# Kernel optimization log

Measured on AMD Instinct MI355X. Metric: run time of the kernel, lower is better.

Reference implementation:

```python
import jax, jax.numpy as jnp
from jax import lax
import numpy as np

B, L, NQ, NL, NC = 2048, 2048, 8, 3, 3  # batch, signal length, qubits, q-layers, classes


def setup_inputs() -> dict:
    key = jax.random.key(0)
    ks = jax.random.split(key, 20)
    rn = lambda k, shape, s=1.0: jax.random.normal(k, shape, jnp.float32) * s
    return dict(
        x_ecg=rn(ks[0], (B, 1, L)), x_eda=rn(ks[1], (B, 1, L)),
        x_emg=rn(ks[2], (B, 1, L)), x_resp=rn(ks[3], (B, 1, L)),
        conv1_w=rn(ks[4], (4, 16, 1, 3), 0.3), conv1_b=rn(ks[5], (4, 16), 0.05),
        conv2_w=rn(ks[6], (4, 32, 16, 3), 0.1), conv2_b=rn(ks[7], (4, 32), 0.05),
        lstm_w_ih=rn(ks[8], (4, 128, 32), 0.1), lstm_w_hh=rn(ks[9], (4, 128, 32), 0.1),
        lstm_b_ih=rn(ks[10], (4, 128), 0.05), lstm_b_hh=rn(ks[11], (4, 128), 0.05),
        bott_w=rn(ks[12], (8, 128), 0.08), bott_b=rn(ks[13], (8,), 0.05),
        q_weights=rn(ks[14], (NL, NQ, 3)),
        clf_w=rn(ks[15], (NC, 8), 0.3), clf_b=rn(ks[16], (NC,), 0.05),
    )


def _branch(x, c1w, c1b, c2w, c2b, wih, whh, bih, bhh):
    # x: [B,1,L]  ->  h_n: [B,32]
    dn = ('NCH', 'OIH', 'NCH')
    h = lax.conv_general_dilated(x, c1w, (1,), [(1, 1)], dimension_numbers=dn) + c1b[None, :, None]
    h = jax.nn.relu(h)
    h = h.reshape(h.shape[0], h.shape[1], -1, 2).max(-1)  # maxpool k=2
    h = lax.conv_general_dilated(h, c2w, (1,), [(1, 1)], dimension_numbers=dn) + c2b[None, :, None]
    h = jax.nn.relu(h)
    h = h.reshape(h.shape[0], h.shape[1], -1, 2).max(-1)  # [B,32,L//4]
    seq = jnp.swapaxes(h, 1, 2)  # [B,T,32]
    Bn, H = seq.shape[0], whh.shape[1]

    def step(carry, xt):
        hprev, cprev = carry
        gates = xt @ wih.T + hprev @ whh.T + bih + bhh  # [B,4H], torch gate order i,f,g,o
        i, f, g, o = jnp.split(gates, 4, axis=-1)
        c = jax.nn.sigmoid(f) * cprev + jax.nn.sigmoid(i) * jnp.tanh(g)
        hn = jax.nn.sigmoid(o) * jnp.tanh(c)
        return (hn, c), None

    init = (jnp.zeros((Bn, H), seq.dtype), jnp.zeros((Bn, H), seq.dtype))
    (h_n, _), _ = lax.scan(step, init, jnp.swapaxes(seq, 0, 1))
    return h_n


def _apply_1q(psi, gate, q, n):
    # psi: [B, 2^n]; gate: [2,2] (shared) or [B,2,2] (per-sample)
    Bn = psi.shape[0]
    left, right = 2 ** q, 2 ** (n - q - 1)
    s = psi.reshape(Bn, left, 2, right)
    if gate.ndim == 2:
        s = jnp.einsum('ij,bljr->blir', gate, s)
    else:
        s = jnp.einsum('bij,bljr->blir', gate, s)
    return s.reshape(Bn, -1)


def _apply_cnot(psi, c, t, n):
    # c < t always here
    Bn = psi.shape[0]
    s = psi.reshape(Bn, 2 ** c, 2, 2 ** (t - c - 1), 2, 2 ** (n - t - 1))
    s = s.at[:, :, 1].set(jnp.flip(s[:, :, 1], axis=3))
    return s.reshape(Bn, -1)


def _rz(a):
    e = jnp.exp(-0.5j * a)
    z = jnp.zeros_like(e)
    return jnp.stack([jnp.stack([e, z]), jnp.stack([z, jnp.conj(e)])])


def _ry(a):
    c, s = jnp.cos(a / 2), jnp.sin(a / 2)
    return jnp.stack([jnp.stack([c, -s]), jnp.stack([s, c])]).astype(jnp.complex64)


def _quantum(compressed, q_weights):
    # batched 8-qubit statevector simulation; compressed: [B, NQ]
    n = NQ
    Bn = compressed.shape[0]
    angles = compressed * jnp.pi
    psi = jnp.zeros((Bn, 2 ** n), jnp.complex64).at[:, 0].set(1.0)
    c, s = jnp.cos(angles / 2), jnp.sin(angles / 2)
    for q in range(n):  # RX embedding, per-sample gates
        g = jnp.stack([jnp.stack([c[:, q], -1j * s[:, q]], -1),
                       jnp.stack([-1j * s[:, q], c[:, q]], -1)], -2)  # [B,2,2]
        psi = _apply_1q(psi, g, q, n)
    for l in range(q_weights.shape[0]):
        for q in range(n):
            w = q_weights[l, q]
            # pennylane Rot(phi,theta,omega) = RZ(omega) @ RY(theta) @ RZ(phi)
            g = _rz(w[2]) @ _ry(w[1]) @ _rz(w[0])
            psi = _apply_1q(psi, g, q, n)
        stride = l + 1
        for q in range(n):
            t = q + stride
            if t < n:
                psi = _apply_cnot(psi, q, t, n)
    p = (jnp.abs(psi) ** 2).reshape((Bn,) + (2,) * n)
    zs = []
    for i in range(n):  # <Z_i> = P(|0>_i) - P(|1>_i)
        axes = tuple(a for a in range(1, n + 1) if a != i + 1)
        m = p.sum(axes)
        zs.append(m[:, 0] - m[:, 1])
    return jnp.stack(zs, -1).astype(jnp.float32)


def reference(x_ecg, x_eda, x_emg, x_resp, conv1_w, conv1_b, conv2_w, conv2_b,
              lstm_w_ih, lstm_w_hh, lstm_b_ih, lstm_b_hh, bott_w, bott_b,
              q_weights, clf_w, clf_b):
    xs = jnp.stack([x_ecg, x_eda, x_emg, x_resp])  # [4,B,1,L]
    feats = jax.vmap(_branch)(xs, conv1_w, conv1_b, conv2_w, conv2_b,
                              lstm_w_ih, lstm_w_hh, lstm_b_ih, lstm_b_hh)  # [4,B,32]
    combined = jnp.transpose(feats, (1, 0, 2)).reshape(feats.shape[1], -1)  # [B,128]
    compressed = jnp.tanh(combined @ bott_w.T + bott_b)  # [B,8]
    q_out = _quantum(compressed, q_weights)  # [B,8]
    logits = q_out @ clf_w.T + clf_b  # [B,3]
    return logits
```

## Files before the change

kernel.cpp:

```cpp
#include <hip/hip_runtime.h>
#include <hip/hip_bf16.h>

#define BATCH 2048
#define LSIG 2048
#define TSTEPS 512
#define CH 16
#define NCHUNK (TSTEPS / CH)

typedef float v2f __attribute__((ext_vector_type(2)));
typedef float v4f __attribute__((ext_vector_type(4)));
typedef __bf16 b16x8 __attribute__((ext_vector_type(8)));
typedef float f32x4 __attribute__((ext_vector_type(4)));

#define PKFMA(d, a, b) asm("v_pk_fma_f32 %0, %1, %2, %0" : "+v"(d) : "v"(a), "v"(b))

__device__ __forceinline__ float sigf(float x) {
    return __fdividef(1.f, 1.f + __expf(-x));
}
__device__ __forceinline__ float tanhfast(float x) {
    return 1.f - __fdividef(2.f, __expf(2.f * x) + 1.f);
}
__device__ __forceinline__ unsigned short bf16rne(float f) {
    unsigned u = __float_as_uint(f);
    return (unsigned short)((u + 0x7FFFu + ((u >> 16) & 1u)) >> 16);
}
__device__ __forceinline__ int swz(int co) {
    return (co < 16) ? ((co >> 2) * 8 + (co & 3))
                     : (((co >> 2) - 4) * 8 + 4 + (co & 3));
}

__global__ __launch_bounds__(64) void frontend_kernel(
    const float* __restrict__ x0, const float* __restrict__ x1,
    const float* __restrict__ x2, const float* __restrict__ x3,
    const float* __restrict__ c1w, const float* __restrict__ c1b,
    const float* __restrict__ c2w, const float* __restrict__ c2b,
    unsigned short* __restrict__ seqh, unsigned short* __restrict__ seql,
    int t0, int Tseg)
{
    const int s    = blockIdx.x;
    const int br   = blockIdx.y & 3;
    const int ck   = blockIdx.y >> 2;
    const int lane = threadIdx.x;
    const float* xg = (br == 0) ? x0 : (br == 1) ? x1 : (br == 2) ? x2 : x3;

    __shared__ float xs_c[70];
    __shared__ float p1buf[34][16];

    const int ci = lane & 15;
    const int co = lane & 31;
    const int hf = lane >> 5;
    const int sp = swz(co);
    const int tc0 = t0 + ck * CH;
    const int lt0 = ck * CH;

    const float w10 = c1w[br * 48 + ci * 3 + 0];
    const float w11 = c1w[br * 48 + ci * 3 + 1];
    const float w12 = c1w[br * 48 + ci * 3 + 2];
    const float b1v = c1b[br * 16 + ci];

    float wt[24];
    {
        const v4f* p = (const v4f*)(c2w + br * 1536 + co * 48 + hf * 24);
        #pragma unroll
        for (int i = 0; i < 6; ++i) ((v4f*)wt)[i] = p[i];
    }
    v4f w2p[3][2];
    #pragma unroll
    for (int k = 0; k < 3; ++k)
        #pragma unroll
        for (int h2 = 0; h2 < 2; ++h2)
            w2p[k][h2] = (v4f){ wt[(h2 * 4 + 0) * 3 + k], wt[(h2 * 4 + 1) * 3 + k],
                                wt[(h2 * 4 + 2) * 3 + k], wt[(h2 * 4 + 3) * 3 + k] };
    const float b2v = c2b[br * 32 + co];

    {
        int g = 4 * tc0 - 3 + lane;
        xs_c[lane] = ((unsigned)g < (unsigned)LSIG) ? xg[(size_t)s * LSIG + g] : 0.f;
        if (lane < 6) {
            int g2 = 4 * tc0 + 61 + lane;
            xs_c[64 + lane] = ((unsigned)g2 < (unsigned)LSIG) ? xg[(size_t)s * LSIG + g2] : 0.f;
        }
    }
    __syncthreads();

    #pragma unroll 1
    for (int it = 0; it < 9; ++it) {
        int idx = it * 64 + lane;
        if (idx < 34 * 16) {
            int pl = idx >> 4;
            float xa = xs_c[2 * pl + 0], xb = xs_c[2 * pl + 1];
            float xc = xs_c[2 * pl + 2], xd = xs_c[2 * pl + 3];
            float a0 = fmaf(xc, w12, fmaf(xb, w11, fmaf(xa, w10, b1v)));
            float a1 = fmaf(xd, w12, fmaf(xc, w11, fmaf(xb, w10, b1v)));
            float v = fmaxf(fmaxf(a0, a1), 0.f);
            int p1g = 2 * tc0 - 1 + pl;
            v = ((unsigned)p1g < (unsigned)(LSIG / 2)) ? v : 0.f;
            p1buf[pl][idx & 15] = v;
        }
    }
    __syncthreads();

    {
        const v4f* pbase = (const v4f*)&p1buf[0][0];
        const int h2o = hf * 2;
        v4f r0a = pbase[0 * 4 + h2o], r0b = pbase[0 * 4 + h2o + 1];
        v4f r1a = pbase[1 * 4 + h2o], r1b = pbase[1 * 4 + h2o + 1];
        v4f r2a = pbase[2 * 4 + h2o], r2b = pbase[2 * 4 + h2o + 1];
        v4f r3a = pbase[3 * 4 + h2o], r3b = pbase[3 * 4 + h2o + 1];
        #pragma unroll 1
        for (int tl = 0; tl < CH; ++tl) {
            v2f aA = {0.f, 0.f}, aB = {0.f, 0.f};
            PKFMA(aA, r0a.xy, w2p[0][0].xy); PKFMA(aA, r0a.zw, w2p[0][0].zw);
            PKFMA(aA, r0b.xy, w2p[0][1].xy); PKFMA(aA, r0b.zw, w2p[0][1].zw);
            PKFMA(aA, r1a.xy, w2p[1][0].xy); PKFMA(aA, r1a.zw, w2p[1][0].zw);
            PKFMA(aA, r1b.xy, w2p[1][1].xy); PKFMA(aA, r1b.zw, w2p[1][1].zw);
            PKFMA(aA, r2a.xy, w2p[2][0].xy); PKFMA(aA, r2a.zw, w2p[2][0].zw);
            PKFMA(aA, r2b.xy, w2p[2][1].xy); PKFMA(aA, r2b.zw, w2p[2][1].zw);
            PKFMA(aB, r1a.xy, w2p[0][0].xy); PKFMA(aB, r1a.zw, w2p[0][0].zw);
            PKFMA(aB, r1b.xy, w2p[0][1].xy); PKFMA(aB, r1b.zw, w2p[0][1].zw);
            PKFMA(aB, r2a.xy, w2p[1][0].xy); PKFMA(aB, r2a.zw, w2p[1][0].zw);
            PKFMA(aB, r2b.xy, w2p[1][1].xy); PKFMA(aB, r2b.zw, w2p[1][1].zw);
            PKFMA(aB, r3a.xy, w2p[2][0].xy); PKFMA(aB, r3a.zw, w2p[2][0].zw);
            PKFMA(aB, r3b.xy, w2p[2][1].xy); PKFMA(aB, r3b.zw, w2p[2][1].zw);
            float sA = aA.x + aA.y, sB = aB.x + aB.y;
            sA += __shfl_xor(sA, 32);
            sB += __shfl_xor(sB, 32);
            float sv = fmaxf(fmaxf(sA, sB) + b2v, 0.f);
            unsigned short hb = bf16rne(sv);
            float hif = __uint_as_float(((unsigned)hb) << 16);
            unsigned short lb = bf16rne(sv - hif);
            size_t off = (((size_t)br * Tseg + (lt0 + tl)) * 2048 + s) * 32 + sp;
            if (hf == 0) seqh[off] = hb;
            else         seql[off] = lb;
            r0a = r2a; r0b = r2b; r1a = r3a; r1b = r3b;
            if (tl < CH - 1) {
                r2a = pbase[(2 * tl + 4) * 4 + h2o]; r2b = pbase[(2 * tl + 4) * 4 + h2o + 1];
                r3a = pbase[(2 * tl + 5) * 4 + h2o]; r3b = pbase[(2 * tl + 5) * 4 + h2o + 1];
            }
        }
    }
}

__global__ __launch_bounds__(64, 1) void lstm_mfma_kernel(
    const unsigned short* __restrict__ seqh, const unsigned short* __restrict__ seql,
    const float* __restrict__ wih, const float* __restrict__ whh,
    const float* __restrict__ bih, const float* __restrict__ bhh,
    float* __restrict__ state, float* __restrict__ feats,
    int t0, int Tseg)
{
    const int s0   = blockIdx.x * 16;
    const int br   = blockIdx.y;
    const int lane = threadIdx.x;
    const int c    = lane & 15;
    const int q    = lane >> 4;

    __shared__ f32x4 bias_lds[8][64];

    #pragma unroll
    for (int n = 0; n < 8; ++n) {
        f32x4 b;
        #pragma unroll
        for (int r = 0; r < 4; ++r) {
            int g = 16 * n + 4 * q + r;
            b[r] = bih[br * 128 + g] + bhh[br * 128 + g];
        }
        bias_lds[n][lane] = b;
    }

    b16x8 wihhi[8], wihlo[8], whhhi[8], whhlo[8];
    #pragma unroll
    for (int n = 0; n < 8; ++n) {
        const int gr = 16 * n + c;
        const float* pi = wih + (size_t)br * 4096 + (size_t)gr * 32;
        const float* ph = whh + (size_t)br * 4096 + (size_t)gr * 32;
        v4f ia = *(const v4f*)(pi + 4 * q);
        v4f ib = *(const v4f*)(pi + 16 + 4 * q);
        v4f ha = *(const v4f*)(ph + 4 * q);
        v4f hb = *(const v4f*)(ph + 16 + 4 * q);
        #pragma unroll
        for (int j = 0; j < 4; ++j) {
            __bf16 t;
            t = (__bf16)ia[j]; wihhi[n][j]     = t; wihlo[n][j]     = (__bf16)(ia[j] - (float)t);
            t = (__bf16)ib[j]; wihhi[n][4 + j] = t; wihlo[n][4 + j] = (__bf16)(ib[j] - (float)t);
            t = (__bf16)ha[j]; whhhi[n][j]     = t; whhlo[n][j]     = (__bf16)(ha[j] - (float)t);
            t = (__bf16)hb[j]; whhhi[n][4 + j] = t; whhlo[n][4 + j] = (__bf16)(hb[j] - (float)t);
        }
    }

    b16x8 bhh_f, bhl_f;
    float cst[2][4];
    if (t0 == 0) {
        #pragma unroll
        for (int j = 0; j < 8; ++j) { bhh_f[j] = (__bf16)0.f; bhl_f[j] = (__bf16)0.f; }
        #pragma unroll
        for (int hh = 0; hh < 2; ++hh)
            #pragma unroll
            for (int r = 0; r < 4; ++r) cst[hh][r] = 0.f;
    } else {
        const float* st = state + (((size_t)br * BATCH + s0 + c) * 2) * 32;
        #pragma unroll
        for (int hh = 0; hh < 2; ++hh)
            #pragma unroll
            for (int r = 0; r < 4; ++r) {
                int u = 16 * hh + 4 * q + r;
                float hv = st[u];
                __bf16 hb2 = (__bf16)hv;
                bhh_f[hh * 4 + r] = hb2;
                bhl_f[hh * 4 + r] = (__bf16)(hv - (float)hb2);
                cst[hh][r] = st[32 + u];
            }
    }
    __syncthreads();

    size_t rowe = (((size_t)br * Tseg + 0) * 2048 + s0 + c) * 32 + (size_t)q * 8;
    b16x8 bxh = *reinterpret_cast<const b16x8*>(seqh + rowe);
    b16x8 bxl = *reinterpret_cast<const b16x8*>(seql + rowe);

    #pragma unroll 1
    for (int t = 0; t < Tseg; ++t) {
        b16x8 nxh = bxh, nxl = bxl;
        if (t < Tseg - 1) {
            size_t re = (((size_t)br * Tseg + (t + 1)) * 2048 + s0 + c) * 32 + (size_t)q * 8;
            nxh = *reinterpret_cast<const b16x8*>(seqh + re);
            nxl = *reinterpret_cast<const b16x8*>(seql + re);
        }

        f32x4 acc[8];
        #pragma unroll
        for (int n = 0; n < 8; ++n) acc[n] = bias_lds[n][lane];
        #pragma unroll
        for (int n = 0; n < 8; ++n) {
            acc[n] = __builtin_amdgcn_mfma_f32_16x16x32_bf16(whhhi[n], bhh_f, acc[n], 0, 0, 0);
            acc[n] = __builtin_amdgcn_mfma_f32_16x16x32_bf16(whhhi[n], bhl_f, acc[n], 0, 0, 0);
            acc[n] = __builtin_amdgcn_mfma_f32_16x16x32_bf16(whhlo[n], bhh_f, acc[n], 0, 0, 0);
            acc[n] = __builtin_amdgcn_mfma_f32_16x16x32_bf16(wihhi[n], bxh,   acc[n], 0, 0, 0);
            acc[n] = __builtin_amdgcn_mfma_f32_16x16x32_bf16(wihhi[n], bxl,   acc[n], 0, 0, 0);
            acc[n] = __builtin_amdgcn_mfma_f32_16x16x32_bf16(wihlo[n], bxh,   acc[n], 0, 0, 0);
        }

        const bool last = (t0 + t == TSTEPS - 1);
        #pragma unroll
        for (int hh = 0; hh < 2; ++hh) {
            #pragma unroll
            for (int r = 0; r < 4; ++r) {
                float gi = acc[0 + hh][r];
                float gf = acc[2 + hh][r];
                float gg = acc[4 + hh][r];
                float go = acc[6 + hh][r];
                float si = sigf(gi);
                float sf = sigf(gf);
                float tg = tanhfast(gg);
                float so = sigf(go);
                float cc = fmaf(sf, cst[hh][r], si * tg);
                cst[hh][r] = cc;
                float hv = so * tanhfast(cc);
                __bf16 hb2 = (__bf16)hv;
                bhh_f[hh * 4 + r] = hb2;
                bhl_f[hh * 4 + r] = (__bf16)(hv - (float)hb2);
                if (last)
                    feats[((size_t)br * BATCH + s0 + c) * 32 + 16 * hh + 4 * q + r] = hv;
            }
        }
        bxh = nxh; bxl = nxl;
    }

    if (t0 + Tseg < TSTEPS) {
        float* st = state + (((size_t)br * BATCH + s0 + c) * 2) * 32;
        #pragma unroll
        for (int hh = 0; hh < 2; ++hh)
            #pragma unroll
            for (int r = 0; r < 4; ++r) {
                int u = 16 * hh + 4 * q + r;
                st[u]      = (float)bhh_f[hh * 4 + r] + (float)bhl_f[hh * 4 + r];
                st[32 + u] = cst[hh][r];
            }
    }
}

__global__ __launch_bounds__(64, 2) void branch_fallback(
    const float* __restrict__ x0, const float* __restrict__ x1,
    const float* __restrict__ x2, const float* __restrict__ x3,
    const float* __restrict__ c1w, const float* __restrict__ c1b,
    const float* __restrict__ c2w, const float* __restrict__ c2b,
    const float* __restrict__ wih, const float* __restrict__ whh,
    const float* __restrict__ bih, const float* __restrict__ bhh,
    float* __restrict__ feats)
{
    const int s    = blockIdx.x;
    const int br   = blockIdx.y;
    const int lane = threadIdx.x;
    const float* xg = (br == 0) ? x0 : (br == 1) ? x1 : (br == 2) ? x2 : x3;

    __shared__ float xs_c[70];
    __shared__ float p1buf[34][16];
    __shared__ float seqb[CH][32];
    __shared__ float hb[2][32];

    const int ci = lane & 15;
    const int co = lane & 31;
    const int hf = lane >> 5;

    const float bs0 = bih[br * 128 + lane]      + bhh[br * 128 + lane];
    const float bs1 = bih[br * 128 + lane + 64] + bhh[br * 128 + lane + 64];

    if (lane < 32) hb[0][lane] = 0.f;
    float c_state = 0.f;

    #pragma unroll 1
    for (int chk = 0; chk < NCHUNK; ++chk) {
        const int tc0 = chk * CH;
        {
            int g = 4 * tc0 - 3 + lane;
            xs_c[lane] = ((unsigned)g < (unsigned)LSIG) ? xg[(size_t)s * LSIG + g] : 0.f;
            if (lane < 6) {
                int g2 = 4 * tc0 + 61 + lane;
                xs_c[64 + lane] = ((unsigned)g2 < (unsigned)LSIG) ? xg[(size_t)s * LSIG + g2] : 0.f;
            }
        }
        const float* pc1 = c1w + br * 48 + ci * 3;  asm volatile("" : "+v"(pc1));
        const float w10 = pc1[0], w11 = pc1[1], w12 = pc1[2];
        const float* pb1 = c1b + br * 16 + ci;      asm volatile("" : "+v"(pb1));
        const float b1v = pb1[0];
        const float* pc2 = c2w + br * 1536 + co * 48 + hf * 24;
        asm volatile("" : "+v"(pc2));
        float wt[24];
        #pragma unroll
        for (int i = 0; i < 6; ++i) ((v4f*)wt)[i] = ((const v4f*)pc2)[i];
        v4f w2p[3][2];
        #pragma unroll
        for (int k = 0; k < 3; ++k)
            #pragma unroll
            for (int h2 = 0; h2 < 2; ++h2)
                w2p[k][h2] = (v4f){ wt[(h2 * 4 + 0) * 3 + k], wt[(h2 * 4 + 1) * 3 + k],
                                    wt[(h2 * 4 + 2) * 3 + k], wt[(h2 * 4 + 3) * 3 + k] };
        const float* pb2 = c2b + br * 32 + co;      asm volatile("" : "+v"(pb2));
        const float b2v = pb2[0];
        __syncthreads();
        #pragma unroll 1
        for (int it = 0; it < 9; ++it) {
            int idx = it * 64 + lane;
            if (idx < 34 * 16) {
                int pl = idx >> 4;
                float xa = xs_c[2 * pl + 0], xb = xs_c[2 * pl + 1];
                float xc = xs_c[2 * pl + 2], xd = xs_c[2 * pl + 3];
                float a0 = fmaf(xc, w12, fmaf(xb, w11, fmaf(xa, w10, b1v)));
                float a1 = fmaf(xd, w12, fmaf(xc, w11, fmaf(xb, w10, b1v)));
                float v = fmaxf(fmaxf(a0, a1), 0.f);
                int p1g = 2 * tc0 - 1 + pl;
                v = ((unsigned)p1g < (unsigned)(LSIG / 2)) ? v : 0.f;
                p1buf[pl][idx & 15] = v;
            }
        }
        __syncthreads();
        {
            const v4f* pbase = (const v4f*)&p1buf[0][0];
            const int h2o = hf * 2;
            v4f r0a = pbase[0 * 4 + h2o], r0b = pbase[0 * 4 + h2o + 1];
            v4f r1a = pbase[1 * 4 + h2o], r1b = pbase[1 * 4 + h2o + 1];
            v4f r2a = pbase[2 * 4 + h2o], r2b = pbase[2 * 4 + h2o + 1];
            v4f r3a = pbase[3 * 4 + h2o], r3b = pbase[3 * 4 + h2o + 1];
            #pragma unroll 1
            for (int tl = 0; tl < CH; ++tl) {
                v2f aA = {0.f, 0.f}, aB = {0.f, 0.f};
                PKFMA(aA, r0a.xy, w2p[0][0].xy); PKFMA(aA, r0a.zw, w2p[0][0].zw);
                PKFMA(aA, r0b.xy, w2p[0][1].xy); PKFMA(aA, r0b.zw, w2p[0][1].zw);
                PKFMA(aA, r1a.xy, w2p[1][0].xy); PKFMA(aA, r1a.zw, w2p[1][0].zw);
                PKFMA(aA, r1b.xy, w2p[1][1].xy); PKFMA(aA, r1b.zw, w2p[1][1].zw);
                PKFMA(aA, r2a.xy, w2p[2][0].xy); PKFMA(aA, r2a.zw, w2p[2][0].zw);
                PKFMA(aA, r2b.xy, w2p[2][1].xy); PKFMA(aA, r2b.zw, w2p[2][1].zw);
                PKFMA(aB, r1a.xy, w2p[0][0].xy); PKFMA(aB, r1a.zw, w2p[0][0].zw);
                PKFMA(aB, r1b.xy, w2p[0][1].xy); PKFMA(aB, r1b.zw, w2p[0][1].zw);
                PKFMA(aB, r2a.xy, w2p[1][0].xy); PKFMA(aB, r2a.zw, w2p[1][0].zw);
                PKFMA(aB, r2b.xy, w2p[1][1].xy); PKFMA(aB, r2b.zw, w2p[1][1].zw);
                PKFMA(aB, r3a.xy, w2p[2][0].xy); PKFMA(aB, r3a.zw, w2p[2][0].zw);
                PKFMA(aB, r3b.xy, w2p[2][1].xy); PKFMA(aB, r3b.zw, w2p[2][1].zw);
                float sA = aA.x + aA.y, sB = aB.x + aB.y;
                sA += __shfl_xor(sA, 32);
                sB += __shfl_xor(sB, 32);
                if (hf == 0)
                    seqb[tl][co] = fmaxf(fmaxf(sA, sB) + b2v, 0.f);
                r0a = r2a; r0b = r2b; r1a = r3a; r1b = r3b;
                if (tl < CH - 1) {
                    r2a = pbase[(2 * tl + 4) * 4 + h2o]; r2b = pbase[(2 * tl + 4) * 4 + h2o + 1];
                    r3a = pbase[(2 * tl + 5) * 4 + h2o]; r3b = pbase[(2 * tl + 5) * 4 + h2o + 1];
                }
            }
        }
        __syncthreads();
        float gpx0[CH], gpx1[CH];
        {
            const float* pwi = wih + (size_t)br * 4096 + (size_t)lane * 32;
            asm volatile("" : "+v"(pwi));
            v4f wiA[8], wiB[8];
            #pragma unroll
            for (int j = 0; j < 8; ++j) {
                wiA[j] = ((const v4f*)pwi)[j];
                wiB[j] = ((const v4f*)(pwi + 64 * 32))[j];
            }
            #pragma unroll
            for (int tl = 0; tl < CH; ++tl) {
                const v4f* xq = (const v4f*)&seqb[tl][0];
                v2f aA = {0.f, 0.f}, aB = {0.f, 0.f};
                #pragma unroll
                for (int j = 0; j < 8; ++j) {
                    v4f xv = xq[j];
                    PKFMA(aA, xv.xy, wiA[j].xy); PKFMA(aA, xv.zw, wiA[j].zw);
                    PKFMA(aB, xv.xy, wiB[j].xy); PKFMA(aB, xv.zw, wiB[j].zw);
                }
                gpx0[tl] = aA.x + aA.y;
                gpx1[tl] = aB.x + aB.y;
            }
        }
        {
            const float* pwh = whh + (size_t)br * 4096 + (size_t)lane * 32;
            asm volatile("" : "+v"(pwh));
            v4f whA[8], whB[8];
            #pragma unroll
            for (int j = 0; j < 8; ++j) {
                whA[j] = ((const v4f*)pwh)[j];
                whB[j] = ((const v4f*)(pwh + 64 * 32))[j];
            }
            #pragma unroll
            for (int tl = 0; tl < CH; ++tl) {
                __syncthreads();
                const int p = (tc0 + tl) & 1;
                const v4f* hq = (const v4f*)&hb[p][0];
                v2f aA = {0.f, 0.f}, aB = {0.f, 0.f};
                #pragma unroll
                for (int j = 0; j < 8; ++j) {
                    v4f hv = hq[j];
                    PKFMA(aA, hv.xy, whA[j].xy); PKFMA(aA, hv.zw, whA[j].zw);
                    PKFMA(aB, hv.xy, whB[j].xy); PKFMA(aB, hv.zw, whB[j].zw);
                }
                float g0 = bs0 + gpx0[tl] + aA.x + aA.y;
                float g1 = bs1 + gpx1[tl] + aB.x + aB.y;
                float a0 = sigf(g0);
                float earg = (lane < 32) ? 2.f * g1 : -g1;
                float e1 = __expf(fminf(earg, 80.f));
                float num = (lane < 32) ? e1 - 1.f : 1.f;
                float a1 = __fdividef(num, e1 + 1.f);
                float fa = __shfl_xor(a0, 32);
                float oa = __shfl_xor(a1, 32);
                if (lane < 32) {
                    c_state = fmaf(fa, c_state, a0 * a1);
                    hb[p ^ 1][lane] = oa * tanhfast(c_state);
                }
            }
        }
    }
    __syncthreads();
    if (lane < 32)
        feats[((size_t)br * BATCH + s) * 32 + lane] = hb[0][lane];
}


__device__ __forceinline__ void apply1q(float2* psi, int lane, int q,
                                        float2 g00, float2 g01,
                                        float2 g10, float2 g11)
{
    const int shift = 7 - q;
    const int right = 1 << shift;
    #pragma unroll
    for (int pp = 0; pp < 2; ++pp) {
        int p  = lane + 64 * pp;
        int l  = p >> shift;
        int r  = p & (right - 1);
        int i0 = (l << (shift + 1)) + r;
        int i1 = i0 + right;
        float2 a = psi[i0], b = psi[i1];
        float2 n0 = make_float2(g00.x * a.x - g00.y * a.y + g01.x * b.x - g01.y * b.y,
                                g00.x * a.y + g00.y * a.x + g01.x * b.y + g01.y * b.x);
        float2 n1 = make_float2(g10.x * a.x - g10.y * a.y + g11.x * b.x - g11.y * b.y,
                                g10.x * a.y + g10.y * a.x + g11.x * b.y + g11.y * b.x);
        psi[i0] = n0;
        psi[i1] = n1;
    }
    __syncthreads();
}

__global__ __launch_bounds__(64) void tail_kernel(
    const float* __restrict__ feats, const float* __restrict__ bw,
    const float* __restrict__ bb, const float* __restrict__ qw,
    const float* __restrict__ cw, const float* __restrict__ cb,
    float* __restrict__ out)
{
    const int s    = blockIdx.x;
    const int lane = threadIdx.x;

    __shared__ float comb[128];
    __shared__ float2 psi[256];
    __shared__ float ang[8];

    comb[lane]      = feats[(size_t)(lane >> 5) * (BATCH * 32) + (size_t)s * 32 + (lane & 31)];
    comb[lane + 64] = feats[(size_t)((lane + 64) >> 5) * (BATCH * 32) + (size_t)s * 32 + (lane & 31)];
    __syncthreads();

    {
        int q = lane >> 3, k0 = lane & 7;
        float p = 0.f;
        #pragma unroll
        for (int i = 0; i < 16; ++i) {
            int k = k0 + 8 * i;
            p = fmaf(comb[k], bw[q * 128 + k], p);
        }
        p += __shfl_xor(p, 4);
        p += __shfl_xor(p, 2);
        p += __shfl_xor(p, 1);
        if (k0 == 0) ang[q] = tanhf(p + bb[q]);
    }
    #pragma unroll
    for (int r = 0; r < 4; ++r) {
        int idx = lane + 64 * r;
        psi[idx] = make_float2(idx == 0 ? 1.f : 0.f, 0.f);
    }
    __syncthreads();

    const float PI_F = 3.14159265358979323846f;

    for (int q = 0; q < 8; ++q) {
        float half = ang[q] * PI_F * 0.5f;
        float cv = cosf(half), sv = sinf(half);
        apply1q(psi, lane, q,
                make_float2(cv, 0.f), make_float2(0.f, -sv),
                make_float2(0.f, -sv), make_float2(cv, 0.f));
    }

    for (int l = 0; l < 3; ++l) {
        for (int q = 0; q < 8; ++q) {
            float phi = qw[(l * 8 + q) * 3 + 0];
            float th  = qw[(l * 8 + q) * 3 + 1];
            float om  = qw[(l * 8 + q) * 3 + 2];
            float ct = cosf(0.5f * th), st = sinf(0.5f * th);
            float A = 0.5f * (phi + om), D = 0.5f * (phi - om);
            float cA = cosf(A), sA = sinf(A), cD = cosf(D), sD = sinf(D);
            apply1q(psi, lane, q,
                    make_float2(ct * cA, -ct * sA), make_float2(-st * cD, -st * sD),
                    make_float2(st * cD, -st * sD), make_float2(ct * cA,  ct * sA));
        }
        int stride = l + 1;
        for (int q = 0; q + stride < 8; ++q) {
            int cbit = 1 << (7 - q);
            int tbit = 1 << (7 - (q + stride));
            #pragma unroll
            for (int r = 0; r < 4; ++r) {
                int idx = lane + 64 * r;
                if ((idx & cbit) && !(idx & tbit)) {
                    int j = idx | tbit;
                    float2 tmp = psi[idx];
                    psi[idx] = psi[j];
                    psi[j] = tmp;
                }
            }
            __syncthreads();
        }
    }

    float z[8];
    #pragma unroll
    for (int q = 0; q < 8; ++q) z[q] = 0.f;
    #pragma unroll
    for (int r = 0; r < 4; ++r) {
        int idx = lane + 64 * r;
        float2 a = psi[idx];
        float pr = a.x * a.x + a.y * a.y;
        #pragma unroll
        for (int q = 0; q < 8; ++q)
            z[q] += (idx & (1 << (7 - q))) ? -pr : pr;
    }
    #pragma unroll
    for (int q = 0; q < 8; ++q) {
        #pragma unroll
        for (int off = 32; off; off >>= 1) z[q] += __shfl_xor(z[q], off);
    }
    if (lane == 0) {
        #pragma unroll
        for (int c = 0; c < 3; ++c) {
            float acc = cb[c];
            #pragma unroll
            for (int q = 0; q < 8; ++q) acc = fmaf(z[q], cw[c * 8 + q], acc);
            out[s * 3 + c] = acc;
        }
    }
}

extern "C" void kernel_launch(void* const* d_in, const int* in_sizes, int n_in,
                              void* d_out, int out_size, void* d_ws, size_t ws_size,
                              hipStream_t stream)
{
    (void)in_sizes; (void)n_in; (void)out_size;
    const float* x0  = (const float*)d_in[0];
    const float* x1  = (const float*)d_in[1];
    const float* x2  = (const float*)d_in[2];
    const float* x3  = (const float*)d_in[3];
    const float* c1w = (const float*)d_in[4];
    const float* c1b = (const float*)d_in[5];
    const float* c2w = (const float*)d_in[6];
    const float* c2b = (const float*)d_in[7];
    const float* wih = (const float*)d_in[8];
    const float* whh = (const float*)d_in[9];
    const float* bih = (const float*)d_in[10];
    const float* bhh = (const float*)d_in[11];
    const float* bw  = (const float*)d_in[12];
    const float* bb  = (const float*)d_in[13];
    const float* qw  = (const float*)d_in[14];
    const float* cw  = (const float*)d_in[15];
    const float* cb  = (const float*)d_in[16];

    const size_t state_b = 4ULL * BATCH * 64ULL * 4ULL;
    const size_t feats_b = 4ULL * BATCH * 32ULL * 4ULL;
    const size_t per_t   = 4ULL * 2048ULL * 32ULL * 4ULL;

    int Tseg = 0;
    for (int cand = 512; cand >= 32; cand >>= 1) {
        if ((size_t)cand * per_t + state_b + feats_b <= ws_size) { Tseg = cand; break; }
    }

    if (Tseg > 0) {
        size_t seg_elems = (size_t)Tseg * 4ULL * 2048ULL * 32ULL;
        unsigned short* seqh = (unsigned short*)d_ws;
        unsigned short* seql = seqh + seg_elems;
        float* state = (float*)((char*)d_ws + 2ULL * seg_elems * 2ULL);
        float* feats = (float*)((char*)state + state_b);

        for (int t0 = 0; t0 < TSTEPS; t0 += Tseg) {
            frontend_kernel<<<dim3(BATCH, 4 * (Tseg / CH)), 64, 0, stream>>>(
                x0, x1, x2, x3, c1w, c1b, c2w, c2b, seqh, seql, t0, Tseg);
            lstm_mfma_kernel<<<dim3(BATCH / 16, 4), 64, 0, stream>>>(
                seqh, seql, wih, whh, bih, bhh, state, feats, t0, Tseg);
        }
        tail_kernel<<<BATCH, 64, 0, stream>>>(
            feats, bw, bb, qw, cw, cb, (float*)d_out);
    } else {
        float* feats = (float*)d_ws;
        branch_fallback<<<dim3(BATCH, 4), 64, 0, stream>>>(
            x0, x1, x2, x3, c1w, c1b, c2w, c2b, wih, whh, bih, bhh, feats);
        tail_kernel<<<BATCH, 64, 0, stream>>>(
            feats, bw, bb, qw, cw, cb, (float*)d_out);
    }
}
```

Baseline: 1.490 ms.

## Split LSTM gate computation across two waves with LDS exchange

Each LSTM block now runs two wavefronts, each owning four of the eight gate tiles. The waves apply their gate activations locally and swap results through double-buffered shared memory with one barrier per step. Both waves then redundantly compute the cell and hidden updates. The input projection for the next step is computed after the current step's update, taking it off the recurrent critical path. This halves the MFMA and transcendental work per wave on the serial recurrence, in exchange for a per-step barrier and extra LDS traffic.

Result: slower. 1.776 ms (+19.2%).

```diff
diff --git a/kernel.cpp b/kernel.cpp
--- a/kernel.cpp
+++ b/kernel.cpp
@@ -141,7 +141,7 @@
     }
 }
 
-__global__ __launch_bounds__(64, 1) void lstm_mfma_kernel(
+__global__ __launch_bounds__(128, 1) void lstm_mfma_kernel(
     const unsigned short* __restrict__ seqh, const unsigned short* __restrict__ seql,
     const float* __restrict__ wih, const float* __restrict__ whh,
     const float* __restrict__ bih, const float* __restrict__ bhh,
@@ -150,26 +150,19 @@
 {
     const int s0   = blockIdx.x * 16;
     const int br   = blockIdx.y;
-    const int lane = threadIdx.x;
+    const int tid  = threadIdx.x;
+    const int w    = tid >> 6;
+    const int lane = tid & 63;
     const int c    = lane & 15;
     const int q    = lane >> 4;
 
-    __shared__ f32x4 bias_lds[8][64];
-
+    __shared__ f32x4 ex[2][2][4][64];
+
+    b16x8 wihhi[4], wihlo[4], whhhi[4], whhlo[4];
+    f32x4 bias[4];
     #pragma unroll
-    for (int n = 0; n < 8; ++n) {
-        f32x4 b;
-        #pragma unroll
-        for (int r = 0; r < 4; ++r) {
-            int g = 16 * n + 4 * q + r;
-            b[r] = bih[br * 128 + g] + bhh[br * 128 + g];
-        }
-        bias_lds[n][lane] = b;
-    }
-
-    b16x8 wihhi[8], wihlo[8], whhhi[8], whhlo[8];
-    #pragma unroll
-    for (int n = 0; n < 8; ++n) {
+    for (int m = 0; m < 4; ++m) {
+        const int n = 4 * w + m;
         const int gr = 16 * n + c;
         const float* pi = wih + (size_t)br * 4096 + (size_t)gr * 32;
         const float* ph = whh + (size_t)br * 4096 + (size_t)gr * 32;
@@ -179,11 +172,16 @@
         v4f hb = *(const v4f*)(ph + 16 + 4 * q);
         #pragma unroll
         for (int j = 0; j < 4; ++j) {
-            __bf16 t;
-            t = (__bf16)ia[j]; wihhi[n][j]     = t; wihlo[n][j]     = (__bf16)(ia[j] - (float)t);
-            t = (__bf16)ib[j]; wihhi[n][4 + j] = t; wihlo[n][4 + j] = (__bf16)(ib[j] - (float)t);
-            t = (__bf16)ha[j]; whhhi[n][j]     = t; whhlo[n][j]     = (__bf16)(ha[j] - (float)t);
-            t = (__bf16)hb[j]; whhhi[n][4 + j] = t; whhlo[n][4 + j] = (__bf16)(hb[j] - (float)t);
+            __bf16 tt;
+            tt = (__bf16)ia[j]; wihhi[m][j]     = tt; wihlo[m][j]     = (__bf16)(ia[j] - (float)tt);
+            tt = (__bf16)ib[j]; wihhi[m][4 + j] = tt; wihlo[m][4 + j] = (__bf16)(ib[j] - (float)tt);
+            tt = (__bf16)ha[j]; whhhi[m][j]     = tt; whhlo[m][j]     = (__bf16)(ha[j] - (float)tt);
+            tt = (__bf16)hb[j]; whhhi[m][4 + j] = tt; whhlo[m][4 + j] = (__bf16)(hb[j] - (float)tt);
+        }
+        #pragma unroll
+        for (int r = 0; r < 4; ++r) {
+            int g = 16 * n + 4 * q + r;
+            bias[m][r] = bih[br * 128 + g] + bhh[br * 128 + g];
         }
     }
 
@@ -210,61 +208,94 @@
                 cst[hh][r] = st[32 + u];
             }
     }
-    __syncthreads();
-
-    size_t rowe = (((size_t)br * Tseg + 0) * 2048 + s0 + c) * 32 + (size_t)q * 8;
-    b16x8 bxh = *reinterpret_cast<const b16x8*>(seqh + rowe);
-    b16x8 bxl = *reinterpret_cast<const b16x8*>(seql + rowe);
+
+    f32x4 xacc[4];
+    {
+        size_t rowe = (((size_t)br * Tseg + 0) * 2048 + s0 + c) * 32 + (size_t)q * 8;
+        b16x8 bxh = *reinterpret_cast<const b16x8*>(seqh + rowe);
+        b16x8 bxl = *reinterpret_cast<const b16x8*>(seql + rowe);
+        #pragma unroll
+        for (int m = 0; m < 4; ++m) {
+            xacc[m] = __builtin_amdgcn_mfma_f32_16x16x32_bf16(wihhi[m], bxh, bias[m], 0, 0, 0);
+            xacc[m] = __builtin_amdgcn_mfma_f32_16x16x32_bf16(wihhi[m], bxl, xacc[m], 0, 0, 0);
+            xacc[m] = __builtin_amdgcn_mfma_f32_16x16x32_bf16(wihlo[m], bxh, xacc[m], 0, 0, 0);
+        }
+    }
 
     #pragma unroll 1
     for (int t = 0; t < Tseg; ++t) {
-        b16x8 nxh = bxh, nxl = bxl;
-        if (t < Tseg - 1) {
+        b16x8 nxh, nxl;
+        const bool more = (t < Tseg - 1);
+        if (more) {
             size_t re = (((size_t)br * Tseg + (t + 1)) * 2048 + s0 + c) * 32 + (size_t)q * 8;
             nxh = *reinterpret_cast<const b16x8*>(seqh + re);
             nxl = *reinterpret_cast<const b16x8*>(seql + re);
         }
 
-        f32x4 acc[8];
-        #pragma unroll
-        for (int n = 0; n < 8; ++n) acc[n] = bias_lds[n][lane];
-        #pragma unroll
-        for (int n = 0; n < 8; ++n) {
-            acc[n] = __builtin_amdgcn_mfma_f32_16x16x32_bf16(whhhi[n], bhh_f, acc[n], 0, 0, 0);
-            acc[n] = __builtin_amdgcn_mfma_f32_16x16x32_bf16(whhhi[n], bhl_f, acc[n], 0, 0, 0);
-            acc[n] = __builtin_amdgcn_mfma_f32_16x16x32_bf16(whhlo[n], bhh_f, acc[n], 0, 0, 0);
-            acc[n] = __builtin_amdgcn_mfma_f32_16x16x32_bf16(wihhi[n], bxh,   acc[n], 0, 0, 0);
-            acc[n] = __builtin_amdgcn_mfma_f32_16x16x32_bf16(wihhi[n], bxl,   acc[n], 0, 0, 0);
-            acc[n] = __builtin_amdgcn_mfma_f32_16x16x32_bf16(wihlo[n], bxh,   acc[n], 0, 0, 0);
-        }
+        f32x4 acc[4];
+        #pragma unroll
+        for (int m = 0; m < 4; ++m) {
+            acc[m] = __builtin_amdgcn_mfma_f32_16x16x32_bf16(whhhi[m], bhh_f, xacc[m], 0, 0, 0);
+            acc[m] = __builtin_amdgcn_mfma_f32_16x16x32_bf16(whhhi[m], bhl_f, acc[m], 0, 0, 0);
+            acc[m] = __builtin_amdgcn_mfma_f32_16x16x32_bf16(whhlo[m], bhh_f, acc[m], 0, 0, 0);
+        }
+
+        f32x4 a[4];
+        if (w == 0) {
+            #pragma unroll
+            for (int m = 0; m < 4; ++m)
+                #pragma unroll
+                for (int r = 0; r < 4; ++r) a[m][r] = sigf(acc[m][r]);
+        } else {
+            #pragma unroll
+            for (int m = 0; m < 2; ++m)
+                #pragma unroll
+                for (int r = 0; r < 4; ++r) a[m][r] = tanhfast(acc[m][r]);
+            #pragma unroll
+            for (int m = 2; m < 4; ++m)
+                #pragma unroll
+                for (int r = 0; r < 4; ++r) a[m][r] = sigf(acc[m][r]);
+        }
+
+        const int par = t & 1;
+        #pragma unroll
+        for (int m = 0; m < 4; ++m) ex[par][w][m][lane] = a[m];
+        __syncthreads();
+        f32x4 ob[4];
+        #pragma unroll
+        for (int m = 0; m < 4; ++m) ob[m] = ex[par][w ^ 1][m][lane];
 
         const bool last = (t0 + t == TSTEPS - 1);
+        const f32x4* P = (w == 0) ? a : ob;
+        const f32x4* Q = (w == 0) ? ob : a;
         #pragma unroll
         for (int hh = 0; hh < 2; ++hh) {
             #pragma unroll
             for (int r = 0; r < 4; ++r) {
-                float gi = acc[0 + hh][r];
-                float gf = acc[2 + hh][r];
-                float gg = acc[4 + hh][r];
-                float go = acc[6 + hh][r];
-                float si = sigf(gi);
-                float sf = sigf(gf);
-                float tg = tanhfast(gg);
-                float so = sigf(go);
-                float cc = fmaf(sf, cst[hh][r], si * tg);
+                float vi = P[hh][r], vf = P[2 + hh][r];
+                float vg = Q[hh][r], vo = Q[2 + hh][r];
+                float cc = fmaf(vf, cst[hh][r], vi * vg);
                 cst[hh][r] = cc;
-                float hv = so * tanhfast(cc);
+                float hv = vo * tanhfast(cc);
                 __bf16 hb2 = (__bf16)hv;
                 bhh_f[hh * 4 + r] = hb2;
                 bhl_f[hh * 4 + r] = (__bf16)(hv - (float)hb2);
-                if (last)
+                if (last && w == 0)
                     feats[((size_t)br * BATCH + s0 + c) * 32 + 16 * hh + 4 * q + r] = hv;
             }
         }
-        bxh = nxh; bxl = nxl;
-    }
-
-    if (t0 + Tseg < TSTEPS) {
+
+        if (more) {
+            #pragma unroll
+            for (int m = 0; m < 4; ++m) {
+                xacc[m] = __builtin_amdgcn_mfma_f32_16x16x32_bf16(wihhi[m], nxh, bias[m], 0, 0, 0);
+                xacc[m] = __builtin_amdgcn_mfma_f32_16x16x32_bf16(wihhi[m], nxl, xacc[m], 0, 0, 0);
+                xacc[m] = __builtin_amdgcn_mfma_f32_16x16x32_bf16(wihlo[m], nxh, xacc[m], 0, 0, 0);
+            }
+        }
+    }
+
+    if (w == 0 && t0 + Tseg < TSTEPS) {
         float* st = state + (((size_t)br * BATCH + s0 + c) * 2) * 32;
         #pragma unroll
         for (int hh = 0; hh < 2; ++hh)
@@ -625,7 +656,7 @@
         for (int t0 = 0; t0 < TSTEPS; t0 += Tseg) {
             frontend_kernel<<<dim3(BATCH, 4 * (Tseg / CH)), 64, 0, stream>>>(
                 x0, x1, x2, x3, c1w, c1b, c2w, c2b, seqh, seql, t0, Tseg);
-            lstm_mfma_kernel<<<dim3(BATCH / 16, 4), 64, 0, stream>>>(
+            lstm_mfma_kernel<<<dim3(BATCH / 16, 4), 128, 0, stream>>>(
                 seqh, seql, wih, whh, bih, bhh, state, feats, t0, Tseg);
         }
         tail_kernel<<<BATCH, 64, 0, stream>>>(
```

## Interleave two independent LSTM batch tiles per wave to overlap MFMA and activations

Applied to the files above, without the earlier changes.

Each LSTM wave now processes two 16-sample tiles instead of one. The MFMA gate chain of one tile is interleaved with the sigmoid/tanh cell update of the other, so matrix and transcendental work from independent recurrences can overlap and hide the serial dependency latency. The grid is halved (BATCH/32 blocks), which lowers wave-level parallelism and raises register pressure with two accumulator sets and two states. The per-gate MFMA order also now puts the input-projection terms before the recurrent ones, so they do not depend on the previous hidden state.

Result: slower. 2.523 ms (+69.4%).

```diff
diff --git a/kernel.cpp b/kernel.cpp
--- a/kernel.cpp
+++ b/kernel.cpp
@@ -141,6 +141,44 @@
     }
 }
 
+#define GATE_CHAINS(ACC, XH, XL, HH, HL)                                        \
+    {                                                                           \
+        _Pragma("unroll")                                                       \
+        for (int n = 0; n < 8; ++n) {                                           \
+            f32x4 a_ = bias_lds[n][lane];                                       \
+            a_ = __builtin_amdgcn_mfma_f32_16x16x32_bf16(wihhi[n], XH, a_, 0, 0, 0); \
+            a_ = __builtin_amdgcn_mfma_f32_16x16x32_bf16(wihhi[n], XL, a_, 0, 0, 0); \
+            a_ = __builtin_amdgcn_mfma_f32_16x16x32_bf16(wihlo[n], XH, a_, 0, 0, 0); \
+            a_ = __builtin_amdgcn_mfma_f32_16x16x32_bf16(whhhi[n], HH, a_, 0, 0, 0); \
+            a_ = __builtin_amdgcn_mfma_f32_16x16x32_bf16(whhhi[n], HL, a_, 0, 0, 0); \
+            a_ = __builtin_amdgcn_mfma_f32_16x16x32_bf16(whhlo[n], HH, a_, 0, 0, 0); \
+            ACC[n] = a_;                                                        \
+        }                                                                       \
+    }
+
+#define ADVANCE(ACC, HH, HL, CS, LAST, FP)                                      \
+    {                                                                           \
+        _Pragma("unroll")                                                       \
+        for (int h2_ = 0; h2_ < 2; ++h2_) {                                     \
+            _Pragma("unroll")                                                   \
+            for (int r_ = 0; r_ < 4; ++r_) {                                    \
+                float gi = ACC[0 + h2_][r_];                                    \
+                float gf = ACC[2 + h2_][r_];                                    \
+                float gg = ACC[4 + h2_][r_];                                    \
+                float go = ACC[6 + h2_][r_];                                    \
+                float si = sigf(gi), sf = sigf(gf);                             \
+                float tg = tanhfast(gg), so = sigf(go);                         \
+                float cc = fmaf(sf, CS[h2_][r_], si * tg);                      \
+                CS[h2_][r_] = cc;                                               \
+                float hv = so * tanhfast(cc);                                   \
+                __bf16 hb2 = (__bf16)hv;                                        \
+                HH[h2_ * 4 + r_] = hb2;                                         \
+                HL[h2_ * 4 + r_] = (__bf16)(hv - (float)hb2);                   \
+                if (LAST) FP[16 * h2_ + 4 * q + r_] = hv;                       \
+            }                                                                   \
+        }                                                                       \
+    }
+
 __global__ __launch_bounds__(64, 1) void lstm_mfma_kernel(
     const unsigned short* __restrict__ seqh, const unsigned short* __restrict__ seql,
     const float* __restrict__ wih, const float* __restrict__ whh,
@@ -148,14 +186,13 @@
     float* __restrict__ state, float* __restrict__ feats,
     int t0, int Tseg)
 {
-    const int s0   = blockIdx.x * 16;
+    const int g0   = blockIdx.x * 32;
     const int br   = blockIdx.y;
     const int lane = threadIdx.x;
     const int c    = lane & 15;
     const int q    = lane >> 4;
 
     __shared__ f32x4 bias_lds[8][64];
-
     #pragma unroll
     for (int n = 0; n < 8; ++n) {
         f32x4 b;
@@ -166,6 +203,7 @@
         }
         bias_lds[n][lane] = b;
     }
+    __syncthreads();
 
     b16x8 wihhi[8], wihlo[8], whhhi[8], whhlo[8];
     #pragma unroll
@@ -179,100 +217,91 @@
         v4f hb = *(const v4f*)(ph + 16 + 4 * q);
         #pragma unroll
         for (int j = 0; j < 4; ++j) {
-            __bf16 t;
-            t = (__bf16)ia[j]; wihhi[n][j]     = t; wihlo[n][j]     = (__bf16)(ia[j] - (float)t);
-            t = (__bf16)ib[j]; wihhi[n][4 + j] = t; wihlo[n][4 + j] = (__bf16)(ib[j] - (float)t);
-            t = (__bf16)ha[j]; whhhi[n][j]     = t; whhlo[n][j]     = (__bf16)(ha[j] - (float)t);
-            t = (__bf16)hb[j]; whhhi[n][4 + j] = t; whhlo[n][4 + j] = (__bf16)(hb[j] - (float)t);
-        }
-    }
-
-    b16x8 bhh_f, bhl_f;
-    float cst[2][4];
+            __bf16 tt;
+            tt = (__bf16)ia[j]; wihhi[n][j]     = tt; wihlo[n][j]     = (__bf16)(ia[j] - (float)tt);
+            tt = (__bf16)ib[j]; wihhi[n][4 + j] = tt; wihlo[n][4 + j] = (__bf16)(ib[j] - (float)tt);
+            tt = (__bf16)ha[j]; whhhi[n][j]     = tt; whhlo[n][j]     = (__bf16)(ha[j] - (float)tt);
+            tt = (__bf16)hb[j]; whhhi[n][4 + j] = tt; whhlo[n][4 + j] = (__bf16)(hb[j] - (float)tt);
+        }
+    }
+
+    b16x8 h0h, h0l, h1h, h1l;
+    float cs0[2][4], cs1[2][4];
     if (t0 == 0) {
         #pragma unroll
-        for (int j = 0; j < 8; ++j) { bhh_f[j] = (__bf16)0.f; bhl_f[j] = (__bf16)0.f; }
-        #pragma unroll
-        for (int hh = 0; hh < 2; ++hh)
-            #pragma unroll
-            for (int r = 0; r < 4; ++r) cst[hh][r] = 0.f;
+        for (int j = 0; j < 8; ++j) {
+            h0h[j] = (__bf16)0.f; h0l[j] = (__bf16)0.f;
+            h1h[j] = (__bf16)0.f; h1l[j] = (__bf16)0.f;
+        }
+        #pragma unroll
+        for (int h2 = 0; h2 < 2; ++h2)
+            #pragma unroll
+            for (int r = 0; r < 4; ++r) { cs0[h2][r] = 0.f; cs1[h2][r] = 0.f; }
     } else {
-        const float* st = state + (((size_t)br * BATCH + s0 + c) * 2) * 32;
-        #pragma unroll
-        for (int hh = 0; hh < 2; ++hh)
+        const float* st0 = state + (((size_t)br * BATCH + g0 + c) * 2) * 32;
+        const float* st1 = state + (((size_t)br * BATCH + g0 + 16 + c) * 2) * 32;
+        #pragma unroll
+        for (int h2 = 0; h2 < 2; ++h2)
             #pragma unroll
             for (int r = 0; r < 4; ++r) {
-                int u = 16 * hh + 4 * q + r;
-                float hv = st[u];
-                __bf16 hb2 = (__bf16)hv;
-                bhh_f[hh * 4 + r] = hb2;
-                bhl_f[hh * 4 + r] = (__bf16)(hv - (float)hb2);
-                cst[hh][r] = st[32 + u];
-            }
-    }
-    __syncthreads();
-
-    size_t rowe = (((size_t)br * Tseg + 0) * 2048 + s0 + c) * 32 + (size_t)q * 8;
-    b16x8 bxh = *reinterpret_cast<const b16x8*>(seqh + rowe);
-    b16x8 bxl = *reinterpret_cast<const b16x8*>(seql + rowe);
+                int u = 16 * h2 + 4 * q + r;
+                float hv0 = st0[u], hv1 = st1[u];
+                __bf16 b0 = (__bf16)hv0, b1 = (__bf16)hv1;
+                h0h[h2 * 4 + r] = b0; h0l[h2 * 4 + r] = (__bf16)(hv0 - (float)b0);
+                h1h[h2 * 4 + r] = b1; h1l[h2 * 4 + r] = (__bf16)(hv1 - (float)b1);
+                cs0[h2][r] = st0[32 + u];
+                cs1[h2][r] = st1[32 + u];
+            }
+    }
+
+    float* fp0 = feats + ((size_t)br * BATCH + g0 + c) * 32;
+    float* fp1 = feats + ((size_t)br * BATCH + g0 + 16 + c) * 32;
+
+    const size_t xbase0 = ((size_t)br * Tseg * 2048 + g0 + c) * 32 + (size_t)q * 8;
+    const size_t xbase1 = xbase0 + 16 * 32;
+    const size_t xstep  = 2048 * 32;
+
+    b16x8 x0h = *(const b16x8*)(seqh + xbase0);
+    b16x8 x0l = *(const b16x8*)(seql + xbase0);
+    f32x4 accA[8], accB[8];
+    {
+        b16x8 p1h = *(const b16x8*)(seqh + xbase1);
+        b16x8 p1l = *(const b16x8*)(seql + xbase1);
+        GATE_CHAINS(accB, p1h, p1l, h1h, h1l);
+    }
 
     #pragma unroll 1
     for (int t = 0; t < Tseg; ++t) {
-        b16x8 nxh = bxh, nxl = bxl;
-        if (t < Tseg - 1) {
-            size_t re = (((size_t)br * Tseg + (t + 1)) * 2048 + s0 + c) * 32 + (size_t)q * 8;
-            nxh = *reinterpret_cast<const b16x8*>(seqh + re);
-            nxl = *reinterpret_cast<const b16x8*>(seql + re);
-        }
-
-        f32x4 acc[8];
-        #pragma unroll
-        for (int n = 0; n < 8; ++n) acc[n] = bias_lds[n][lane];
-        #pragma unroll
-        for (int n = 0; n < 8; ++n) {
-            acc[n] = __builtin_amdgcn_mfma_f32_16x16x32_bf16(whhhi[n], bhh_f, acc[n], 0, 0, 0);
-            acc[n] = __builtin_amdgcn_mfma_f32_16x16x32_bf16(whhhi[n], bhl_f, acc[n], 0, 0, 0);
-            acc[n] = __builtin_amdgcn_mfma_f32_16x16x32_bf16(whhlo[n], bhh_f, acc[n], 0, 0, 0);
-            acc[n] = __builtin_amdgcn_mfma_f32_16x16x32_bf16(wihhi[n], bxh,   acc[n], 0, 0, 0);
-            acc[n] = __builtin_amdgcn_mfma_f32_16x16x32_bf16(wihhi[n], bxl,   acc[n], 0, 0, 0);
-            acc[n] = __builtin_amdgcn_mfma_f32_16x16x32_bf16(wihlo[n], bxh,   acc[n], 0, 0, 0);
-        }
-
+        const bool more = (t < Tseg - 1);
         const bool last = (t0 + t == TSTEPS - 1);
-        #pragma unroll
-        for (int hh = 0; hh < 2; ++hh) {
+        b16x8 n0h, n0l, n1h, n1l;
+        if (more) {
+            size_t r0 = xbase0 + (size_t)(t + 1) * xstep;
+            size_t r1 = xbase1 + (size_t)(t + 1) * xstep;
+            n0h = *(const b16x8*)(seqh + r0); n0l = *(const b16x8*)(seql + r0);
+            n1h = *(const b16x8*)(seqh + r1); n1l = *(const b16x8*)(seql + r1);
+        }
+
+        GATE_CHAINS(accA, x0h, x0l, h0h, h0l);
+        ADVANCE(accB, h1h, h1l, cs1, last, fp1);
+        if (more) { GATE_CHAINS(accB, n1h, n1l, h1h, h1l); }
+        ADVANCE(accA, h0h, h0l, cs0, last, fp0);
+
+        x0h = n0h; x0l = n0l;
+    }
+
+    if (t0 + Tseg < TSTEPS) {
+        float* st0 = state + (((size_t)br * BATCH + g0 + c) * 2) * 32;
+        float* st1 = state + (((size_t)br * BATCH + g0 + 16 + c) * 2) * 32;
+        #pragma unroll
+        for (int h2 = 0; h2 < 2; ++h2)
             #pragma unroll
             for (int r = 0; r < 4; ++r) {
-                float gi = acc[0 + hh][r];
-                float gf = acc[2 + hh][r];
-                float gg = acc[4 + hh][r];
-                float go = acc[6 + hh][r];
-                float si = sigf(gi);
-                float sf = sigf(gf);
-                float tg = tanhfast(gg);
-                float so = sigf(go);
-                float cc = fmaf(sf, cst[hh][r], si * tg);
-                cst[hh][r] = cc;
-                float hv = so * tanhfast(cc);
-                __bf16 hb2 = (__bf16)hv;
-                bhh_f[hh * 4 + r] = hb2;
-                bhl_f[hh * 4 + r] = (__bf16)(hv - (float)hb2);
-                if (last)
-                    feats[((size_t)br * BATCH + s0 + c) * 32 + 16 * hh + 4 * q + r] = hv;
-            }
-        }
-        bxh = nxh; bxl = nxl;
-    }
-
-    if (t0 + Tseg < TSTEPS) {
-        float* st = state + (((size_t)br * BATCH + s0 + c) * 2) * 32;
-        #pragma unroll
-        for (int hh = 0; hh < 2; ++hh)
-            #pragma unroll
-            for (int r = 0; r < 4; ++r) {
-                int u = 16 * hh + 4 * q + r;
-                st[u]      = (float)bhh_f[hh * 4 + r] + (float)bhl_f[hh * 4 + r];
-                st[32 + u] = cst[hh][r];
+                int u = 16 * h2 + 4 * q + r;
+                st0[u]      = (float)h0h[h2 * 4 + r] + (float)h0l[h2 * 4 + r];
+                st0[32 + u] = cs0[h2][r];
+                st1[u]      = (float)h1h[h2 * 4 + r] + (float)h1l[h2 * 4 + r];
+                st1[32 + u] = cs1[h2][r];
             }
     }
 }
@@ -625,7 +654,7 @@
         for (int t0 = 0; t0 < TSTEPS; t0 += Tseg) {
             frontend_kernel<<<dim3(BATCH, 4 * (Tseg / CH)), 64, 0, stream>>>(
                 x0, x1, x2, x3, c1w, c1b, c2w, c2b, seqh, seql, t0, Tseg);
-            lstm_mfma_kernel<<<dim3(BATCH / 16, 4), 64, 0, stream>>>(
+            lstm_mfma_kernel<<<dim3(BATCH / 32, 4), 64, 0, stream>>>(
                 seqh, seql, wih, whh, bih, bhh, state, feats, t0, Tseg);
         }
         tail_kernel<<<BATCH, 64, 0, stream>>>(
```

## Precompute next-step input projection off the LSTM recurrence critical path

Applied to the files above, without the earlier changes.

Moves the input-to-hidden MFMAs for step t+1 to after the gate nonlinearities of step t, so only the three hidden-state MFMAs per gate tile sit on the serial dependency chain. The input prefetch is deepened to two steps ahead. The bias is now held in registers instead of LDS, which removes the per-step LDS reads and the __syncthreads. This costs extra VGPRs for the bias and prefetch buffers, which may raise register pressure under launch_bounds(64,1).

New measurement: 1.535 ms. 1.03x slower.

```diff
diff --git a/kernel.cpp b/kernel.cpp
--- a/kernel.cpp
+++ b/kernel.cpp
@@ -154,18 +154,14 @@
     const int c    = lane & 15;
     const int q    = lane >> 4;
 
-    __shared__ f32x4 bias_lds[8][64];
-
-    #pragma unroll
-    for (int n = 0; n < 8; ++n) {
-        f32x4 b;
+    f32x4 bias[8];
+    #pragma unroll
+    for (int n = 0; n < 8; ++n)
         #pragma unroll
         for (int r = 0; r < 4; ++r) {
             int g = 16 * n + 4 * q + r;
-            b[r] = bih[br * 128 + g] + bhh[br * 128 + g];
-        }
-        bias_lds[n][lane] = b;
-    }
+            bias[n][r] = bih[br * 128 + g] + bhh[br * 128 + g];
+        }
 
     b16x8 wihhi[8], wihlo[8], whhhi[8], whhlo[8];
     #pragma unroll
@@ -210,43 +206,51 @@
                 cst[hh][r] = st[32 + u];
             }
     }
-    __syncthreads();
-
-    size_t rowe = (((size_t)br * Tseg + 0) * 2048 + s0 + c) * 32 + (size_t)q * 8;
-    b16x8 bxh = *reinterpret_cast<const b16x8*>(seqh + rowe);
-    b16x8 bxl = *reinterpret_cast<const b16x8*>(seql + rowe);
+
+    const size_t xbase = ((size_t)br * Tseg * 2048 + s0 + c) * 32 + (size_t)q * 8;
+    const size_t xstep = 2048 * 32;
+    const unsigned short* ph = seqh + xbase;
+    const unsigned short* pl = seql + xbase;
+
+    f32x4 xacc[8];
+    b16x8 nh1, nl1;
+    {
+        b16x8 x0h = *(const b16x8*)ph;
+        b16x8 x0l = *(const b16x8*)pl;
+        #pragma unroll
+        for (int n = 0; n < 8; ++n) {
+            xacc[n] = __builtin_amdgcn_mfma_f32_16x16x32_bf16(wihhi[n], x0h, bias[n], 0, 0, 0);
+            xacc[n] = __builtin_amdgcn_mfma_f32_16x16x32_bf16(wihhi[n], x0l, xacc[n], 0, 0, 0);
+            xacc[n] = __builtin_amdgcn_mfma_f32_16x16x32_bf16(wihlo[n], x0h, xacc[n], 0, 0, 0);
+        }
+        nh1 = *(const b16x8*)(ph + xstep);
+        nl1 = *(const b16x8*)(pl + xstep);
+    }
 
     #pragma unroll 1
     for (int t = 0; t < Tseg; ++t) {
-        b16x8 nxh = bxh, nxl = bxl;
-        if (t < Tseg - 1) {
-            size_t re = (((size_t)br * Tseg + (t + 1)) * 2048 + s0 + c) * 32 + (size_t)q * 8;
-            nxh = *reinterpret_cast<const b16x8*>(seqh + re);
-            nxl = *reinterpret_cast<const b16x8*>(seql + re);
-        }
-
-        f32x4 acc[8];
-        #pragma unroll
-        for (int n = 0; n < 8; ++n) acc[n] = bias_lds[n][lane];
+        const bool last = (t0 + t == TSTEPS - 1);
+        b16x8 nh2, nl2;
+        if (t + 2 < Tseg) {
+            nh2 = *(const b16x8*)(ph + (size_t)(t + 2) * xstep);
+            nl2 = *(const b16x8*)(pl + (size_t)(t + 2) * xstep);
+        }
+
         #pragma unroll
         for (int n = 0; n < 8; ++n) {
-            acc[n] = __builtin_amdgcn_mfma_f32_16x16x32_bf16(whhhi[n], bhh_f, acc[n], 0, 0, 0);
-            acc[n] = __builtin_amdgcn_mfma_f32_16x16x32_bf16(whhhi[n], bhl_f, acc[n], 0, 0, 0);
-            acc[n] = __builtin_amdgcn_mfma_f32_16x16x32_bf16(whhlo[n], bhh_f, acc[n], 0, 0, 0);
-            acc[n] = __builtin_amdgcn_mfma_f32_16x16x32_bf16(wihhi[n], bxh,   acc[n], 0, 0, 0);
-            acc[n] = __builtin_amdgcn_mfma_f32_16x16x32_bf16(wihhi[n], bxl,   acc[n], 0, 0, 0);
-            acc[n] = __builtin_amdgcn_mfma_f32_16x16x32_bf16(wihlo[n], bxh,   acc[n], 0, 0, 0);
-        }
-
-        const bool last = (t0 + t == TSTEPS - 1);
+            xacc[n] = __builtin_amdgcn_mfma_f32_16x16x32_bf16(whhhi[n], bhh_f, xacc[n], 0, 0, 0);
+            xacc[n] = __builtin_amdgcn_mfma_f32_16x16x32_bf16(whhhi[n], bhl_f, xacc[n], 0, 0, 0);
+            xacc[n] = __builtin_amdgcn_mfma_f32_16x16x32_bf16(whhlo[n], bhh_f, xacc[n], 0, 0, 0);
+        }
+
         #pragma unroll
         for (int hh = 0; hh < 2; ++hh) {
             #pragma unroll
             for (int r = 0; r < 4; ++r) {
-                float gi = acc[0 + hh][r];
-                float gf = acc[2 + hh][r];
-                float gg = acc[4 + hh][r];
-                float go = acc[6 + hh][r];
+                float gi = xacc[0 + hh][r];
+                float gf = xacc[2 + hh][r];
+                float gg = xacc[4 + hh][r];
+                float go = xacc[6 + hh][r];
                 float si = sigf(gi);
                 float sf = sigf(gf);
                 float tg = tanhfast(gg);
@@ -261,7 +265,16 @@
                     feats[((size_t)br * BATCH + s0 + c) * 32 + 16 * hh + 4 * q + r] = hv;
             }
         }
-        bxh = nxh; bxl = nxl;
+
+        if (t < Tseg - 1) {
+            #pragma unroll
+            for (int n = 0; n < 8; ++n) {
+                xacc[n] = __builtin_amdgcn_mfma_f32_16x16x32_bf16(wihhi[n], nh1, bias[n], 0, 0, 0);
+                xacc[n] = __builtin_amdgcn_mfma_f32_16x16x32_bf16(wihhi[n], nl1, xacc[n], 0, 0, 0);
+                xacc[n] = __builtin_amdgcn_mfma_f32_16x16x32_bf16(wihlo[n], nh1, xacc[n], 0, 0, 0);
+            }
+            nh1 = nh2; nl1 = nl2;
+        }
     }
 
     if (t0 + Tseg < TSTEPS) {
```
